# Performance work log

Measured on AMD Instinct MI355X. Metric: run time of the kernel, lower is better.

## Reference

```python
import jax, jax.numpy as jnp
import numpy as np

EMBED_DIM = 1024
NUM_HEADS = 16
HEAD_DIM = EMBED_DIM // NUM_HEADS
SEQ_LEN = 2048
BATCH = 2
THETA_BASE = 10000.0


def rope_angles(head_dim, max_seq_len):
    inv_freq = 1.0 / (THETA_BASE ** (jnp.arange(0, head_dim, 2, dtype=jnp.float32) / head_dim))
    pos = jnp.arange(max_seq_len, dtype=jnp.float32)
    angles = pos[:, None] * inv_freq[None, :]              # [S, D/2]
    angles = jnp.concatenate([angles, angles], axis=-1)    # [S, D]
    return jnp.cos(angles), jnp.sin(angles)


def apply_rope(x, cos, sin):
    # x: [B, H, S, D]; cos/sin: [S, D]
    d = x.shape[-1]
    x1, x2 = x[..., : d // 2], x[..., d // 2 :]
    rotated = jnp.concatenate([-x2, x1], axis=-1)
    return x * cos[None, None, :, :] + rotated * sin[None, None, :, :]


def setup_inputs() -> dict:
    key = jax.random.key(0)
    kx, kq, kk, kv, ko = jax.random.split(key, 5)
    s = 1.0 / np.sqrt(EMBED_DIM)
    return {
        "x": jax.random.normal(kx, (BATCH, SEQ_LEN, EMBED_DIM), dtype=jnp.float32),
        "Wq": jax.random.normal(kq, (EMBED_DIM, EMBED_DIM), dtype=jnp.float32) * s,
        "Wk": jax.random.normal(kk, (EMBED_DIM, EMBED_DIM), dtype=jnp.float32) * s,
        "Wv": jax.random.normal(kv, (EMBED_DIM, EMBED_DIM), dtype=jnp.float32) * s,
        "Wo": jax.random.normal(ko, (EMBED_DIM, EMBED_DIM), dtype=jnp.float32) * s,
    }


def reference(x, Wq, Wk, Wv, Wo):
    B, S, E = x.shape
    H, D = NUM_HEADS, HEAD_DIM
    cos, sin = rope_angles(D, S)

    def split_heads(t):
        return t.reshape(B, S, H, D).transpose(0, 2, 1, 3)  # [B,H,S,D]

    q = split_heads(x @ Wq.T)
    k = split_heads(x @ Wk.T)
    v = split_heads(x @ Wv.T)

    q = apply_rope(q, cos, sin)
    k = apply_rope(k, cos, sin)

    scores = jnp.einsum("bhsd,bhtd->bhst", q, k)
    causal = jnp.triu(jnp.ones((S, S), dtype=bool), k=1)
    scores = jnp.where(causal[None, None, :, :], -jnp.inf, scores)
    weights = jax.nn.softmax(scores / jnp.sqrt(jnp.float32(D)), axis=-1)

    ctx = jnp.einsum("bhst,bhtd->bhsd", weights, v)
    ctx = ctx.transpose(0, 2, 1, 3).reshape(B, S, E)
    return ctx @ Wo.T
```

## Files before the change

### kernel.cpp

```cpp
#include <hip/hip_runtime.h>
#include <hip/hip_bf16.h>

#define H_NUM 16
#define D_DIM 64
#define S_LEN 2048
#define EMB   1024
#define M_TOT 4096

typedef unsigned short u16;
typedef unsigned int   u32;
typedef __attribute__((ext_vector_type(8))) short short8;
typedef __attribute__((ext_vector_type(4))) float f32x4;

__device__ __forceinline__ u32 f2bf_u(float f) {
    u32 u = __float_as_uint(f);
    return (u + 0x7fffu + ((u >> 16) & 1u)) >> 16;
}
__device__ __forceinline__ u32 pack2(float a, float b) {
    return f2bf_u(a) | (f2bf_u(b) << 16);
}
__device__ __forceinline__ u32 pack2t(float a, float b) {
    return __builtin_amdgcn_perm(__float_as_uint(b), __float_as_uint(a),
                                 0x07060302u);
}
__device__ __forceinline__ uint4 pack8(float4 lo, float4 hi) {
    return make_uint4(pack2(lo.x, lo.y), pack2(lo.z, lo.w),
                      pack2(hi.x, hi.y), pack2(hi.z, hi.w));
}

__device__ __forceinline__ void lds_dma16(const u16* g, u16* l) {
    __builtin_amdgcn_global_load_lds(
        (const __attribute__((address_space(1))) void*)g,
        (__attribute__((address_space(3))) void*)l, 16, 0, 0);
}

__global__ __launch_bounds__(256) void cast_kernel(
    const float* __restrict__ x,  const float* __restrict__ Wq,
    const float* __restrict__ Wk, const float* __restrict__ Wv,
    const float* __restrict__ Wo, u16* __restrict__ ws, float2* __restrict__ tab)
{
    const int seg = blockIdx.y;
    if (seg == 5) {
        const int idx = blockIdx.x * 256 + threadIdx.x;
        if (idx < S_LEN * 32) {
            const int s = idx >> 5, d = idx & 31;
            const float ang = (float)s * __expf(-(float)d * 0.28782313662425573f);
            tab[idx] = make_float2(cosf(ang), sinf(ang));
        }
        return;
    }
    const float* src = (seg == 0) ? x : (seg == 1) ? Wq : (seg == 2) ? Wk
                     : (seg == 3) ? Wv : Wo;
    u16* dst = (seg == 0) ? ws : ws + (3 + seg) * 1048576;
    const int n = (seg == 0) ? 4194304 : 1048576;
    const int idx = (blockIdx.x * 256 + threadIdx.x) * 8;
    if (idx < n) {
        float4 lo = *(const float4*)(src + idx);
        float4 hi = *(const float4*)(src + idx + 4);
        *(uint4*)(dst + idx) = pack8(lo, hi);
    }
}

__global__ __launch_bounds__(256) void qkv_rope_kernel(
    const u16* __restrict__ xb, const u16* __restrict__ wb,
    const float2* __restrict__ tab,
    u16* __restrict__ qo, u16* __restrict__ ko, u16* __restrict__ vo)
{
    const int w  = blockIdx.y >> 3;
    const int nb = blockIdx.y & 7;
    const u16* W = wb + w * 1048576;

    __shared__ __align__(16) u16 smem[12288];
    u16* As = smem;
    u16* Bs = smem + 64 * 64;
    u16 (*Ep)[132] = (u16(*)[132])smem;

    const int tid   = threadIdx.x;
    const int lane  = tid & 63;
    const int wid   = tid >> 6;
    const int waveM = wid >> 1;
    const int waveN = wid & 1;
    const int col16 = lane & 15;
    const int quad  = lane >> 4;

    const int m0 = blockIdx.x * 64;
    const int n0 = nb * 128;

    f32x4 acc[2][4];
    const f32x4 zero4 = {0.f, 0.f, 0.f, 0.f};
#pragma unroll
    for (int i = 0; i < 2; i++)
#pragma unroll
        for (int j = 0; j < 4; j++) acc[i][j] = zero4;

    const int drow = tid >> 3;
    const int dpos = tid & 7;
    const u16* Ag = xb + (size_t)m0 * EMB;
    const u16* Bg = W  + (size_t)n0 * EMB;

    for (int k0 = 0; k0 < EMB; k0 += 64) {
        __syncthreads();
#pragma unroll
        for (int j = 0; j < 2; j++) {
            const int rl = j * 32 + drow;
            const int cg = dpos ^ (rl & 7);
            lds_dma16(Ag + (size_t)rl * EMB + k0 + cg * 8,
                      As + (j * 32 + wid * 8) * 64);
        }
#pragma unroll
        for (int j = 0; j < 4; j++) {
            const int rl = j * 32 + drow;
            const int cg = dpos ^ (rl & 7);
            lds_dma16(Bg + (size_t)rl * EMB + k0 + cg * 8,
                      Bs + (j * 32 + wid * 8) * 64);
        }
        __syncthreads();

        short8 af[2][2], bf[4][2];
#pragma unroll
        for (int mt = 0; mt < 2; mt++) {
            const int r = waveM * 32 + mt * 16 + col16;
#pragma unroll
            for (int ks = 0; ks < 2; ks++) {
                const int p = (ks * 4 + quad) ^ (r & 7);
                af[mt][ks] = *(const short8*)(As + r * 64 + p * 8);
            }
        }
#pragma unroll
        for (int nt = 0; nt < 4; nt++) {
            const int r = waveN * 64 + nt * 16 + col16;
#pragma unroll
            for (int ks = 0; ks < 2; ks++) {
                const int p = (ks * 4 + quad) ^ (r & 7);
                bf[nt][ks] = *(const short8*)(Bs + r * 64 + p * 8);
            }
        }
#pragma unroll
        for (int ks = 0; ks < 2; ks++)
#pragma unroll
            for (int mt = 0; mt < 2; mt++)
#pragma unroll
                for (int nt = 0; nt < 4; nt++)
                    acc[mt][nt] = __builtin_amdgcn_mfma_f32_16x16x32_bf16(
                        af[mt][ks], bf[nt][ks], acc[mt][nt], 0, 0, 0);
    }

    const float qs = (w == 0) ? 0.18033688011112042f : 1.0f;
    __syncthreads();
#pragma unroll
    for (int mt = 0; mt < 2; mt++) {
#pragma unroll
        for (int r = 0; r < 4; r++) {
            const int m_local = waveM * 32 + mt * 16 + quad * 4 + r;
            const int s = (m0 + m_local) & 2047;
            if (w == 2) {
#pragma unroll
                for (int nt = 0; nt < 4; nt++)
                    Ep[m_local][waveN * 64 + nt * 16 + col16] =
                        (u16)f2bf_u(acc[mt][nt][r]);
            } else {
#pragma unroll
                for (int nt = 0; nt < 2; nt++) {
                    const int d = nt * 16 + col16;
                    const float2 cs = tab[s * 32 + d];
                    const float lo = acc[mt][nt][r];
                    const float hi = acc[mt][nt + 2][r];
                    Ep[m_local][waveN * 64 + d]      =
                        (u16)f2bf_u((lo * cs.x - hi * cs.y) * qs);
                    Ep[m_local][waveN * 64 + d + 32] =
                        (u16)f2bf_u((hi * cs.x + lo * cs.y) * qs);
                }
            }
        }
    }
    __syncthreads();

    const int b = m0 >> 11;
    if (w != 2) {
        u16* out = (w == 0) ? qo : ko;
#pragma unroll
        for (int j = 0; j < 4; j++) {
            const int g = j * 256 + tid;
            const int head_local = g >> 9;
            const int sl  = (g >> 3) & 63;
            const int cir = g & 7;
            uint4 val = *(const uint4*)(&Ep[sl][head_local * 64 + cir * 8]);
            const int h = (n0 >> 6) + head_local;
            const size_t base = (((size_t)(b * H_NUM + h)) * S_LEN + (m0 & 2047)) * 64;
            *(uint4*)(out + base + (size_t)(g & 511) * 8) = val;
        }
    } else {
        const int s0 = m0 & 2047;
#pragma unroll
        for (int j = 0; j < 4; j++) {
            const int g = j * 256 + tid;
            const int d_all = g >> 3;
            const int sc = g & 7;
            u32 wv[4];
#pragma unroll
            for (int hw = 0; hw < 4; hw++) {
                const int p0 = sc * 8 + hw * 2;
                const int r0 = ((p0 & 3) << 4) | (p0 >> 2);
                const int p1 = p0 + 1;
                const int r1 = ((p1 & 3) << 4) | (p1 >> 2);
                wv[hw] = (u32)Ep[r0][d_all] | ((u32)Ep[r1][d_all] << 16);
            }
            const int h = (n0 >> 6) + (d_all >> 6);
            const int d = d_all & 63;
            *(uint4*)(vo + ((size_t)(b * H_NUM + h) * 64 + d) * 2048 + s0 + sc * 8) =
                make_uint4(wv[0], wv[1], wv[2], wv[3]);
        }
    }
}

__global__ __launch_bounds__(512) void attn_kernel(
    const u16* __restrict__ q, const u16* __restrict__ k,
    const u16* __restrict__ v, u16* __restrict__ ctx)
{
    __shared__ __align__(16) u16 QPA[64 * 64];
    __shared__ __align__(16) u16 QPB[64 * 64];
    __shared__ __align__(16) u16 Ks[2][2][64 * 64];
    __shared__ __align__(16) u16 VTs[2][2][64 * 64];

    const int tid   = threadIdx.x;
    const int lane  = tid & 63;
    const int wid   = tid >> 6;
    const int w4    = wid & 3;
    const bool isB  = (wid >= 4);
    const int col16 = lane & 15;
    const int quad  = lane >> 4;

    const int bh = blockIdx.x;
    const int p  = blockIdx.y;
    const int qbA = p;
    const int qbB = 31 - p;
    const int myQb   = isB ? qbB : qbA;
    const int myBase = myQb * 64;
    const size_t bhOff = (size_t)bh * S_LEN * D_DIM;

    const int srow = tid >> 3;
    const int spos = tid & 7;
    const int scg  = spos ^ (srow & 7);

    u16* qdst = isB ? QPB : QPA;

    auto stage = [&](int kt, int buf, int slot) {
        lds_dma16(k + bhOff + (size_t)(kt * 64 + srow) * 64 + scg * 8,
                  &Ks[buf][slot][wid * 512]);
        lds_dma16(v + bhOff + (size_t)srow * 2048 + kt * 64 + scg * 8,
                  &VTs[buf][slot][wid * 512]);
    };

    stage(0, 0, 0);
    stage(1, 0, 1);
    {
        const int r5 = srow & 31;
#pragma unroll
        for (int j = 0; j < 2; j++) {
            const int rl = j * 32 + r5;
            const int cg = spos ^ (rl & 7);
            lds_dma16(q + bhOff + (size_t)(myBase + rl) * 64 + cg * 8,
                      qdst + (j * 32 + w4 * 8) * 64);
        }
    }
    __syncthreads();

    short8 qf[2];
    {
        const int rq = w4 * 16 + col16;
#pragma unroll
        for (int ks = 0; ks < 2; ks++) {
            const int c = (ks * 4 + quad) ^ (rq & 7);
            qf[ks] = *(const short8*)(qdst + rq * 64 + c * 8);
        }
    }

    const short ONE = (short)0x3F80;
    const short8 onesf = {ONE, ONE, ONE, ONE, ONE, ONE, ONE, ONE};

    f32x4 O[4];
    const f32x4 zero4 = {0.f, 0.f, 0.f, 0.f};
#pragma unroll
    for (int j = 0; j < 4; j++) O[j] = zero4;
    f32x4 lacc = zero4;

    int buf = 0;
    for (int kt0 = 0; kt0 <= qbB; kt0 += 2) {
        if (kt0 > 0) __syncthreads();
        if (kt0 + 2 <= qbB) {
            stage(kt0 + 2, buf ^ 1, 0);
            if (kt0 + 3 <= qbB) stage(kt0 + 3, buf ^ 1, 1);
        }

#pragma unroll
        for (int sl = 0; sl < 2; sl++) {
            const int kt = kt0 + sl;
            if (kt > qbB || kt > myQb) continue;

            f32x4 sc[4];
#pragma unroll
            for (int nt = 0; nt < 4; nt++) sc[nt] = zero4;
#pragma unroll
            for (int ks = 0; ks < 2; ks++) {
                short8 kf[4];
#pragma unroll
                for (int nt = 0; nt < 4; nt++) {
                    const int rk = nt * 16 + col16;
                    const int c = (ks * 4 + quad) ^ (rk & 7);
                    kf[nt] = *(const short8*)(&Ks[buf][sl][rk * 64 + c * 8]);
                }
                __builtin_amdgcn_s_setprio(1);
#pragma unroll
                for (int nt = 0; nt < 4; nt++)
                    sc[nt] = __builtin_amdgcn_mfma_f32_16x16x32_bf16(
                        qf[ks], kf[nt], sc[nt], 0, 0, 0);
                __builtin_amdgcn_s_setprio(0);
            }

            if (kt == myQb) {
#pragma unroll
                for (int r = 0; r < 4; r++) {
                    const int qg = myBase + w4 * 16 + quad * 4 + r;
#pragma unroll
                    for (int nt = 0; nt < 4; nt++) {
                        const int kg = kt * 64 + nt * 16 + col16;
                        float pv = __builtin_amdgcn_exp2f(sc[nt][r]);
                        if (kg > qg) pv = 0.f;
                        sc[nt][r] = pv;
                    }
                }
            } else {
#pragma unroll
                for (int r = 0; r < 4; r++)
#pragma unroll
                    for (int nt = 0; nt < 4; nt++)
                        sc[nt][r] = __builtin_amdgcn_exp2f(sc[nt][r]);
            }

#pragma unroll
            for (int r = 0; r < 4; r++) {
                const int ml = quad * 4 + r;
                const u32 lo = pack2t(sc[0][r], sc[1][r]);
                const u32 hi = pack2t(sc[2][r], sc[3][r]);
                *(uint2*)(qdst + (w4 * 16 + ml) * 64 +
                          (((col16 >> 1) ^ (ml & 7)) * 8 + (col16 & 1) * 4)) =
                    make_uint2(lo, hi);
            }

#pragma unroll
            for (int ks = 0; ks < 2; ks++) {
                short8 pf, vf[4];
                {
                    const int c = (ks * 4 + quad) ^ (col16 & 7);
                    pf = *(const short8*)(qdst + (w4 * 16 + col16) * 64 + c * 8);
                }
#pragma unroll
                for (int dt = 0; dt < 4; dt++) {
                    const int d = dt * 16 + col16;
                    const int c = (ks * 4 + quad) ^ (d & 7);
                    vf[dt] = *(const short8*)(&VTs[buf][sl][d * 64 + c * 8]);
                }
                __builtin_amdgcn_s_setprio(1);
#pragma unroll
                for (int dt = 0; dt < 4; dt++)
                    O[dt] = __builtin_amdgcn_mfma_f32_16x16x32_bf16(
                        pf, vf[dt], O[dt], 0, 0, 0);
                lacc = __builtin_amdgcn_mfma_f32_16x16x32_bf16(
                    pf, onesf, lacc, 0, 0, 0);
                __builtin_amdgcn_s_setprio(0);
            }
        }
        buf ^= 1;
    }

    const int b = bh >> 4, h = bh & 15;
#pragma unroll
    for (int r = 0; r < 4; r++) {
        const int ml = quad * 4 + r;
        const float inv = __builtin_amdgcn_rcpf(lacc[r]);
        const u32 lo = pack2t(O[0][r] * inv, O[1][r] * inv);
        const u32 hi = pack2t(O[2][r] * inv, O[3][r] * inv);
        *(uint2*)(qdst + (w4 * 16 + ml) * 64 +
                  (((col16 >> 1) ^ (ml & 7)) * 8 + (col16 & 1) * 4)) =
            make_uint2(lo, hi);
    }
#pragma unroll
    for (int j = 0; j < 2; j++) {
        const int gg  = j * 64 + lane;
        const int sl = gg >> 3;
        const int cir = gg & 7;
        u32 wv[4];
#pragma unroll
        for (int hw = 0; hw < 4; hw++) {
            const int d0 = cir * 8 + hw * 2;
            const int p0 = ((d0 & 15) << 2) | (d0 >> 4);
            const int d1 = d0 + 1;
            const int p1 = ((d1 & 15) << 2) | (d1 >> 4);
            const u16 v0 = qdst[(w4 * 16 + sl) * 64 + ((p0 >> 3) ^ (sl & 7)) * 8 + (p0 & 7)];
            const u16 v1 = qdst[(w4 * 16 + sl) * 64 + ((p1 >> 3) ^ (sl & 7)) * 8 + (p1 & 7)];
            wv[hw] = (u32)v0 | ((u32)v1 << 16);
        }
        const size_t rowbase =
            ((size_t)b * S_LEN + myBase + w4 * 16 + sl) * EMB + h * 64;
        *(uint4*)(ctx + rowbase + cir * 8) = make_uint4(wv[0], wv[1], wv[2], wv[3]);
    }
}

__global__ __launch_bounds__(256) void proj_kernel(
    const u16* __restrict__ X, const u16* __restrict__ W, float* __restrict__ out)
{
    __shared__ __align__(16) u16 smem[16384];

    const int tid   = threadIdx.x;
    const int lane  = tid & 63;
    const int wid   = tid >> 6;
    const int col16 = lane & 15;
    const int quad  = lane >> 4;

    const int m0 = blockIdx.x * 64;
    const int n0 = blockIdx.y * 64;

    u16* As = smem;
    u16* Bs = smem + 64 * 128;

    f32x4 acc[4];
    const f32x4 zero4 = {0.f, 0.f, 0.f, 0.f};
#pragma unroll
    for (int i = 0; i < 4; i++) acc[i] = zero4;

    const int srow4 = lane >> 4;
    const int pos   = lane & 15;
    const u16* Ag = X + (size_t)m0 * EMB;
    const u16* Bg = W + (size_t)n0 * EMB;

    for (int kk = 0; kk < 8; kk++) {
        const int k0 = kk * 128;
        __syncthreads();
#pragma unroll
        for (int jj = 0; jj < 4; jj++) {
            const int row = jj * 16 + wid * 4 + srow4;
            const int cg = (pos & 8) | ((pos & 7) ^ (row & 7));
            lds_dma16(Ag + (size_t)row * EMB + k0 + cg * 8,
                      As + (jj * 16 + wid * 4) * 128);
        }
#pragma unroll
        for (int jj = 0; jj < 4; jj++) {
            const int row = jj * 16 + wid * 4 + srow4;
            const int cg = (pos & 8) | ((pos & 7) ^ (row & 7));
            lds_dma16(Bg + (size_t)row * EMB + k0 + cg * 8,
                      Bs + (jj * 16 + wid * 4) * 128);
        }
        __syncthreads();

#pragma unroll
        for (int half = 0; half < 2; half++) {
            short8 af[2], bf[4][2];
            {
                const int r = wid * 16 + col16;
#pragma unroll
                for (int ks = 0; ks < 2; ks++) {
                    const int p = half * 8 + (((ks * 4 + quad)) ^ (r & 7));
                    af[ks] = *(const short8*)(As + r * 128 + p * 8);
                }
            }
#pragma unroll
            for (int nt = 0; nt < 4; nt++) {
                const int r = nt * 16 + col16;
#pragma unroll
                for (int ks = 0; ks < 2; ks++) {
                    const int p = half * 8 + (((ks * 4 + quad)) ^ (r & 7));
                    bf[nt][ks] = *(const short8*)(Bs + r * 128 + p * 8);
                }
            }
#pragma unroll
            for (int ks = 0; ks < 2; ks++)
#pragma unroll
                for (int nt = 0; nt < 4; nt++)
                    acc[nt] = __builtin_amdgcn_mfma_f32_16x16x32_bf16(
                        bf[nt][ks], af[ks], acc[nt], 0, 0, 0);
        }
    }

#pragma unroll
    for (int nt = 0; nt < 4; nt++) {
        const int m_g = m0 + wid * 16 + col16;
        const int n_g = n0 + nt * 16 + quad * 4;
        *(f32x4*)(out + (size_t)m_g * EMB + n_g) = acc[nt];
    }
}

extern "C" void kernel_launch(void* const* d_in, const int* in_sizes, int n_in,
                              void* d_out, int out_size, void* d_ws, size_t ws_size,
                              hipStream_t stream)
{
    const float* x  = (const float*)d_in[0];
    const float* Wq = (const float*)d_in[1];
    const float* Wk = (const float*)d_in[2];
    const float* Wv = (const float*)d_in[3];
    const float* Wo = (const float*)d_in[4];

    u16* ws = (u16*)d_ws;
    u16* xb  = ws;
    u16* wb  = ws + 4194304;
    u16* wob = ws + 7340032;
    u16* q   = ws + 8388608;
    u16* k   = ws + 12582912;
    u16* v   = ws + 16777216;
    u16* ctx = ws + 20971520;
    float2* tab = (float2*)(ws + 25165824);

    cast_kernel<<<dim3(2048, 6), 256, 0, stream>>>(x, Wq, Wk, Wv, Wo, ws, tab);
    qkv_rope_kernel<<<dim3(64, 24), 256, 0, stream>>>(xb, wb, tab, q, k, v);
    attn_kernel<<<dim3(32, 16), 512, 0, stream>>>(q, k, v, ctx);
    proj_kernel<<<dim3(64, 16), 256, 0, stream>>>(ctx, wob, (float*)d_out);
}
```

Before: 160.5 us.

## Split attention KV tiles across wave groups and merge partial outputs via LDS

Previously each group of four waves owned one query block (A or B) and walked all key tiles for it, so the A group idled once its causal range ended. Now each wave group takes alternating key tiles (even or odd slot) and processes both query blocks for those tiles. The groups then exchange partial O and row-sum accumulators through the reused K/V shared buffers before normalising. This balances work between the two wave groups at the cost of doubled accumulator registers, an extra reduction step with two barriers, and a launch_bounds occupancy hint.

```diff
diff --git a/kernel.cpp b/kernel.cpp
--- a/kernel.cpp
+++ b/kernel.cpp
@@ -213,12 +213,11 @@
     }
 }
 
-__global__ __launch_bounds__(512) void attn_kernel(
+__global__ __launch_bounds__(512, 4) void attn_kernel(
     const u16* __restrict__ q, const u16* __restrict__ k,
     const u16* __restrict__ v, u16* __restrict__ ctx)
 {
-    __shared__ __align__(16) u16 QPA[64 * 64];
-    __shared__ __align__(16) u16 QPB[64 * 64];
+    __shared__ __align__(16) u16 QP[2][64 * 64];
     __shared__ __align__(16) u16 Ks[2][2][64 * 64];
     __shared__ __align__(16) u16 VTs[2][2][64 * 64];
 
@@ -226,7 +225,7 @@
     const int lane  = tid & 63;
     const int wid   = tid >> 6;
     const int w4    = wid & 3;
-    const bool isB  = (wid >= 4);
+    const int g     = wid >> 2;
     const int col16 = lane & 15;
     const int quad  = lane >> 4;
 
@@ -234,15 +233,13 @@
     const int p  = blockIdx.y;
     const int qbA = p;
     const int qbB = 31 - p;
-    const int myQb   = isB ? qbB : qbA;
-    const int myBase = myQb * 64;
+    const int qBaseA = qbA * 64;
+    const int qBaseB = qbB * 64;
     const size_t bhOff = (size_t)bh * S_LEN * D_DIM;
 
     const int srow = tid >> 3;
     const int spos = tid & 7;
     const int scg  = spos ^ (srow & 7);
-
-    u16* qdst = isB ? QPB : QPA;
 
     auto stage = [&](int kt, int buf, int slot) {
         lds_dma16(k + bhOff + (size_t)(kt * 64 + srow) * 64 + scg * 8,
@@ -254,133 +251,169 @@
     stage(0, 0, 0);
     stage(1, 0, 1);
     {
+        const int stBase = g ? qBaseB : qBaseA;
         const int r5 = srow & 31;
 #pragma unroll
         for (int j = 0; j < 2; j++) {
             const int rl = j * 32 + r5;
             const int cg = spos ^ (rl & 7);
-            lds_dma16(q + bhOff + (size_t)(myBase + rl) * 64 + cg * 8,
-                      qdst + (j * 32 + w4 * 8) * 64);
+            lds_dma16(q + bhOff + (size_t)(stBase + rl) * 64 + cg * 8,
+                      QP[g] + (j * 32 + w4 * 8) * 64);
         }
     }
     __syncthreads();
 
-    short8 qf[2];
+    short8 qfA[2], qfB[2];
     {
         const int rq = w4 * 16 + col16;
 #pragma unroll
         for (int ks = 0; ks < 2; ks++) {
             const int c = (ks * 4 + quad) ^ (rq & 7);
-            qf[ks] = *(const short8*)(qdst + rq * 64 + c * 8);
-        }
-    }
+            qfA[ks] = *(const short8*)(QP[0] + rq * 64 + c * 8);
+            qfB[ks] = *(const short8*)(QP[1] + rq * 64 + c * 8);
+        }
+    }
+
+    u16* myP = ((u16*)QP) + wid * 1024;
 
     const short ONE = (short)0x3F80;
     const short8 onesf = {ONE, ONE, ONE, ONE, ONE, ONE, ONE, ONE};
 
-    f32x4 O[4];
+    f32x4 OA[4], OB[4];
     const f32x4 zero4 = {0.f, 0.f, 0.f, 0.f};
 #pragma unroll
-    for (int j = 0; j < 4; j++) O[j] = zero4;
-    f32x4 lacc = zero4;
+    for (int j = 0; j < 4; j++) { OA[j] = zero4; OB[j] = zero4; }
+    f32x4 laccA = zero4, laccB = zero4;
+
+    auto proc = [&](const short8* qf, f32x4* O, f32x4& lacc,
+                    int qBase, int qb, int kt, int bufv) {
+        const int sl = g;
+        f32x4 sc[4];
+#pragma unroll
+        for (int nt = 0; nt < 4; nt++) sc[nt] = zero4;
+#pragma unroll
+        for (int ks = 0; ks < 2; ks++) {
+            short8 kf[4];
+#pragma unroll
+            for (int nt = 0; nt < 4; nt++) {
+                const int rk = nt * 16 + col16;
+                const int c = (ks * 4 + quad) ^ (rk & 7);
+                kf[nt] = *(const short8*)(&Ks[bufv][sl][rk * 64 + c * 8]);
+            }
+            __builtin_amdgcn_s_setprio(1);
+#pragma unroll
+            for (int nt = 0; nt < 4; nt++)
+                sc[nt] = __builtin_amdgcn_mfma_f32_16x16x32_bf16(
+                    qf[ks], kf[nt], sc[nt], 0, 0, 0);
+            __builtin_amdgcn_s_setprio(0);
+        }
+
+        if (kt == qb) {
+#pragma unroll
+            for (int r = 0; r < 4; r++) {
+                const int qg = qBase + w4 * 16 + quad * 4 + r;
+#pragma unroll
+                for (int nt = 0; nt < 4; nt++) {
+                    const int kg = kt * 64 + nt * 16 + col16;
+                    float pv = __builtin_amdgcn_exp2f(sc[nt][r]);
+                    if (kg > qg) pv = 0.f;
+                    sc[nt][r] = pv;
+                }
+            }
+        } else {
+#pragma unroll
+            for (int r = 0; r < 4; r++)
+#pragma unroll
+                for (int nt = 0; nt < 4; nt++)
+                    sc[nt][r] = __builtin_amdgcn_exp2f(sc[nt][r]);
+        }
+
+#pragma unroll
+        for (int r = 0; r < 4; r++) {
+            const int ml = quad * 4 + r;
+            const u32 lo = pack2t(sc[0][r], sc[1][r]);
+            const u32 hi = pack2t(sc[2][r], sc[3][r]);
+            *(uint2*)(myP + ml * 64 +
+                      (((col16 >> 1) ^ (ml & 7)) * 8 + (col16 & 1) * 4)) =
+                make_uint2(lo, hi);
+        }
+
+#pragma unroll
+        for (int ks = 0; ks < 2; ks++) {
+            short8 pf, vf[4];
+            {
+                const int c = (ks * 4 + quad) ^ (col16 & 7);
+                pf = *(const short8*)(myP + col16 * 64 + c * 8);
+            }
+#pragma unroll
+            for (int dt = 0; dt < 4; dt++) {
+                const int d = dt * 16 + col16;
+                const int c = (ks * 4 + quad) ^ (d & 7);
+                vf[dt] = *(const short8*)(&VTs[bufv][sl][d * 64 + c * 8]);
+            }
+            __builtin_amdgcn_s_setprio(1);
+#pragma unroll
+            for (int dt = 0; dt < 4; dt++)
+                O[dt] = __builtin_amdgcn_mfma_f32_16x16x32_bf16(
+                    pf, vf[dt], O[dt], 0, 0, 0);
+            lacc = __builtin_amdgcn_mfma_f32_16x16x32_bf16(
+                pf, onesf, lacc, 0, 0, 0);
+            __builtin_amdgcn_s_setprio(0);
+        }
+    };
 
     int buf = 0;
     for (int kt0 = 0; kt0 <= qbB; kt0 += 2) {
-        if (kt0 > 0) __syncthreads();
+        __syncthreads();
         if (kt0 + 2 <= qbB) {
             stage(kt0 + 2, buf ^ 1, 0);
             if (kt0 + 3 <= qbB) stage(kt0 + 3, buf ^ 1, 1);
         }
-
-#pragma unroll
-        for (int sl = 0; sl < 2; sl++) {
-            const int kt = kt0 + sl;
-            if (kt > qbB || kt > myQb) continue;
-
-            f32x4 sc[4];
-#pragma unroll
-            for (int nt = 0; nt < 4; nt++) sc[nt] = zero4;
-#pragma unroll
-            for (int ks = 0; ks < 2; ks++) {
-                short8 kf[4];
-#pragma unroll
-                for (int nt = 0; nt < 4; nt++) {
-                    const int rk = nt * 16 + col16;
-                    const int c = (ks * 4 + quad) ^ (rk & 7);
-                    kf[nt] = *(const short8*)(&Ks[buf][sl][rk * 64 + c * 8]);
-                }
-                __builtin_amdgcn_s_setprio(1);
-#pragma unroll
-                for (int nt = 0; nt < 4; nt++)
-                    sc[nt] = __builtin_amdgcn_mfma_f32_16x16x32_bf16(
-                        qf[ks], kf[nt], sc[nt], 0, 0, 0);
-                __builtin_amdgcn_s_setprio(0);
-            }
-
-            if (kt == myQb) {
-#pragma unroll
-                for (int r = 0; r < 4; r++) {
-                    const int qg = myBase + w4 * 16 + quad * 4 + r;
-#pragma unroll
-                    for (int nt = 0; nt < 4; nt++) {
-                        const int kg = kt * 64 + nt * 16 + col16;
-                        float pv = __builtin_amdgcn_exp2f(sc[nt][r]);
-                        if (kg > qg) pv = 0.f;
-                        sc[nt][r] = pv;
-                    }
-                }
-            } else {
-#pragma unroll
-                for (int r = 0; r < 4; r++)
-#pragma unroll
-                    for (int nt = 0; nt < 4; nt++)
-                        sc[nt][r] = __builtin_amdgcn_exp2f(sc[nt][r]);
-            }
-
-#pragma unroll
-            for (int r = 0; r < 4; r++) {
-                const int ml = quad * 4 + r;
-                const u32 lo = pack2t(sc[0][r], sc[1][r]);
-                const u32 hi = pack2t(sc[2][r], sc[3][r]);
-                *(uint2*)(qdst + (w4 * 16 + ml) * 64 +
-                          (((col16 >> 1) ^ (ml & 7)) * 8 + (col16 & 1) * 4)) =
-                    make_uint2(lo, hi);
-            }
-
-#pragma unroll
-            for (int ks = 0; ks < 2; ks++) {
-                short8 pf, vf[4];
-                {
-                    const int c = (ks * 4 + quad) ^ (col16 & 7);
-                    pf = *(const short8*)(qdst + (w4 * 16 + col16) * 64 + c * 8);
-                }
-#pragma unroll
-                for (int dt = 0; dt < 4; dt++) {
-                    const int d = dt * 16 + col16;
-                    const int c = (ks * 4 + quad) ^ (d & 7);
-                    vf[dt] = *(const short8*)(&VTs[buf][sl][d * 64 + c * 8]);
-                }
-                __builtin_amdgcn_s_setprio(1);
-#pragma unroll
-                for (int dt = 0; dt < 4; dt++)
-                    O[dt] = __builtin_amdgcn_mfma_f32_16x16x32_bf16(
-                        pf, vf[dt], O[dt], 0, 0, 0);
-                lacc = __builtin_amdgcn_mfma_f32_16x16x32_bf16(
-                    pf, onesf, lacc, 0, 0, 0);
-                __builtin_amdgcn_s_setprio(0);
-            }
+        const int kt = kt0 + g;
+        if (kt <= qbB) {
+            proc(qfB, OB, laccB, qBaseB, qbB, kt, buf);
+            if (kt <= qbA)
+                proc(qfA, OA, laccA, qBaseA, qbA, kt, buf);
         }
         buf ^= 1;
     }
 
+    __syncthreads();
+    {
+        float* eb = (g ? (float*)&VTs[0][0][0] : (float*)&Ks[0][0][0])
+                    + w4 * 1296;
+        f32x4* eO = g ? OA : OB;
+        f32x4  eL = g ? laccA : laccB;
+#pragma unroll
+        for (int dt = 0; dt < 4; dt++)
+            *(f32x4*)(eb + lane * 20 + dt * 4) = eO[dt];
+        if (col16 == 0)
+            *(f32x4*)(eb + 1280 + quad * 4) = eL;
+    }
+    __syncthreads();
+    f32x4 myO[4];
+    f32x4 myL;
+    {
+        float* ib = (g ? (float*)&Ks[0][0][0] : (float*)&VTs[0][0][0])
+                    + w4 * 1296;
+#pragma unroll
+        for (int dt = 0; dt < 4; dt++) {
+            const f32x4 pp = *(const f32x4*)(ib + lane * 20 + dt * 4);
+            myO[dt] = (g ? OB[dt] : OA[dt]) + pp;
+        }
+        const f32x4 lp = *(const f32x4*)(ib + 1280 + quad * 4);
+        myL = (g ? laccB : laccA) + lp;
+    }
+
     const int b = bh >> 4, h = bh & 15;
+    const int outBase = g ? qBaseB : qBaseA;
 #pragma unroll
     for (int r = 0; r < 4; r++) {
         const int ml = quad * 4 + r;
-        const float inv = __builtin_amdgcn_rcpf(lacc[r]);
-        const u32 lo = pack2t(O[0][r] * inv, O[1][r] * inv);
-        const u32 hi = pack2t(O[2][r] * inv, O[3][r] * inv);
-        *(uint2*)(qdst + (w4 * 16 + ml) * 64 +
+        const float inv = __builtin_amdgcn_rcpf(myL[r]);
+        const u32 lo = pack2t(myO[0][r] * inv, myO[1][r] * inv);
+        const u32 hi = pack2t(myO[2][r] * inv, myO[3][r] * inv);
+        *(uint2*)(myP + ml * 64 +
                   (((col16 >> 1) ^ (ml & 7)) * 8 + (col16 & 1) * 4)) =
             make_uint2(lo, hi);
     }
@@ -396,12 +429,12 @@
             const int p0 = ((d0 & 15) << 2) | (d0 >> 4);
             const int d1 = d0 + 1;
             const int p1 = ((d1 & 15) << 2) | (d1 >> 4);
-            const u16 v0 = qdst[(w4 * 16 + sl) * 64 + ((p0 >> 3) ^ (sl & 7)) * 8 + (p0 & 7)];
-            const u16 v1 = qdst[(w4 * 16 + sl) * 64 + ((p1 >> 3) ^ (sl & 7)) * 8 + (p1 & 7)];
+            const u16 v0 = myP[sl * 64 + ((p0 >> 3) ^ (sl & 7)) * 8 + (p0 & 7)];
+            const u16 v1 = myP[sl * 64 + ((p1 >> 3) ^ (sl & 7)) * 8 + (p1 & 7)];
             wv[hw] = (u32)v0 | ((u32)v1 << 16);
         }
         const size_t rowbase =
-            ((size_t)b * S_LEN + myBase + w4 * 16 + sl) * EMB + h * 64;
+            ((size_t)b * S_LEN + outBase + w4 * 16 + sl) * EMB + h * 64;
         *(uint4*)(ctx + rowbase + cir * 8) = make_uint4(wv[0], wv[1], wv[2], wv[3]);
     }
 }
```

New measurement: 158.8 us. About the same (-1.0%).
